# Kernel optimization log

Hardware: AMD Instinct MI355X
Metric: run time of the kernel (lower is better)

Reference implementation:

```python
import jax, jax.numpy as jnp
import numpy as np

D_IN = 4096
NUM_HEADS = 32
NUM_KV_GROUPS = 8
HEAD_DIM = D_IN // NUM_HEADS  # 128 (init overwrites head_dim)
GROUP_SIZE = NUM_HEADS // NUM_KV_GROUPS
SEQ = 2048
BATCH = 1
EPS = 1e-6


def layernorm(t, w, b):
    mu = jnp.mean(t, axis=-1, keepdims=True)
    var = jnp.var(t, axis=-1, keepdims=True)
    return (t - mu) * jax.lax.rsqrt(var + EPS) * w + b


def rope(t, cos, sin):
    # t: [B, H, S, D]; cos/sin: [S, D] broadcast over B, H
    half = t.shape[-1] // 2
    x1, x2 = t[..., :half], t[..., half:]
    rot = jnp.concatenate([-x2, x1], axis=-1)
    return t * cos + rot * sin


def setup_inputs() -> dict:
    key = jax.random.key(0)
    ks = jax.random.split(key, 10)
    x = jax.random.normal(ks[0], (BATCH, SEQ, D_IN), dtype=jnp.float32)
    mask = jnp.triu(jnp.ones((SEQ, SEQ), dtype=bool), k=1)  # True = masked (causal)
    # RoPE tables
    inv_freq = 1.0 / (10000.0 ** (np.arange(0, HEAD_DIM, 2, dtype=np.float32) / HEAD_DIM))
    pos = np.arange(SEQ, dtype=np.float32)
    ang = np.einsum('s,d->sd', pos, inv_freq)  # [S, D/2]
    ang = np.concatenate([ang, ang], axis=-1)  # [S, D]
    cos = jnp.asarray(np.cos(ang))
    sin = jnp.asarray(np.sin(ang))
    s = 0.02
    Wq = jax.random.normal(ks[1], (D_IN, NUM_HEADS * HEAD_DIM), dtype=jnp.float32) * s
    Wk = jax.random.normal(ks[2], (D_IN, NUM_KV_GROUPS * HEAD_DIM), dtype=jnp.float32) * s
    Wv = jax.random.normal(ks[3], (D_IN, NUM_KV_GROUPS * HEAD_DIM), dtype=jnp.float32) * s
    Wo = jax.random.normal(ks[4], (NUM_HEADS * HEAD_DIM, D_IN), dtype=jnp.float32) * s
    qn_w = jnp.ones((HEAD_DIM,), jnp.float32)
    qn_b = jnp.zeros((HEAD_DIM,), jnp.float32)
    kn_w = jnp.ones((HEAD_DIM,), jnp.float32)
    kn_b = jnp.zeros((HEAD_DIM,), jnp.float32)
    return {"x": x, "mask": mask, "cos": cos, "sin": sin, "Wq": Wq, "Wk": Wk,
            "Wv": Wv, "Wo": Wo, "qn_w": qn_w, "qn_b": qn_b, "kn_w": kn_w, "kn_b": kn_b}


def reference(x, mask, cos, sin, Wq, Wk, Wv, Wo, qn_w, qn_b, kn_w, kn_b):
    B, S, _ = x.shape
    q = (x @ Wq).reshape(B, S, NUM_HEADS, HEAD_DIM).transpose(0, 2, 1, 3)      # [B,H,S,D]
    k = (x @ Wk).reshape(B, S, NUM_KV_GROUPS, HEAD_DIM).transpose(0, 2, 1, 3)  # [B,G,S,D]
    v = (x @ Wv).reshape(B, S, NUM_KV_GROUPS, HEAD_DIM).transpose(0, 2, 1, 3)
    q = layernorm(q, qn_w, qn_b)
    k = layernorm(k, kn_w, kn_b)
    q = rope(q, cos, sin)
    k = rope(k, cos, sin)
    k = jnp.repeat(k, GROUP_SIZE, axis=1)  # [B,H,S,D]
    v = jnp.repeat(v, GROUP_SIZE, axis=1)
    scores = jnp.einsum('bhqd,bhkd->bhqk', q, k)
    scores = jnp.where(mask, -jnp.inf, scores)
    attn = jax.nn.softmax(scores / jnp.sqrt(jnp.float32(HEAD_DIM)), axis=-1)
    ctx = jnp.einsum('bhqk,bhkd->bhqd', attn, v)
    ctx = ctx.transpose(0, 2, 1, 3).reshape(B, S, NUM_HEADS * HEAD_DIM)
    return ctx @ Wo
```

## Files before the change

kernel.cpp:

```cpp
#include <hip/hip_runtime.h>
#include <stdint.h>

#define SQ   2048
#define DIN  4096
#define NH   32
#define NKV  8
#define HD   128
#define NQKV 6144

typedef float f32x4 __attribute__((ext_vector_type(4)));
typedef short bf16x8 __attribute__((ext_vector_type(8)));

__device__ __forceinline__ short f2bf(float f) {
  union { float f; uint32_t u; } v; v.f = f;
  uint32_t r = (v.u + 0x7FFFu + ((v.u >> 16) & 1u)) >> 16;
  return (short)r;
}

__device__ __forceinline__ void gl2lds(const void* g, void* l) {
  __builtin_amdgcn_global_load_lds(
      (const __attribute__((address_space(1))) void*)g,
      (__attribute__((address_space(3))) void*)l, 16, 0, 0);
}

__global__ void cvt_bf16(const float* __restrict__ src, short* __restrict__ dst, long n) {
  long i = ((long)blockIdx.x * blockDim.x + threadIdx.x) * 4;
  if (i + 3 < n) {
    float4 v = *(const float4*)(src + i);
    short o[4] = { f2bf(v.x), f2bf(v.y), f2bf(v.z), f2bf(v.w) };
    *(uint2*)(dst + i) = *(uint2*)o;
  }
}

__global__ __launch_bounds__(256) void transpose_cvt(const float* __restrict__ src, int ldS, long zS,
                                                     short* __restrict__ dst, int ldD, long zD) {
  __shared__ float tile[64][65];
  src += (long)blockIdx.z * zS;
  dst += (long)blockIdx.z * zD;
  int r0 = blockIdx.y * 64, c0 = blockIdx.x * 64;
  int tid = threadIdx.x;
#pragma unroll
  for (int i = 0; i < 16; ++i) {
    int idx = i * 256 + tid;
    int rr = idx >> 6, cc = idx & 63;
    tile[rr][cc] = src[(long)(r0 + rr) * ldS + c0 + cc];
  }
  __syncthreads();
#pragma unroll
  for (int i = 0; i < 16; ++i) {
    int idx = i * 256 + tid;
    int dr = idx >> 6, dc = idx & 63;
    dst[(long)(c0 + dr) * ldD + r0 + dc] = f2bf(tile[dc][dr]);
  }
}

#define HBUF  8192
#define BUFSZ 32768
#define MFMA(d, a, b) d = __builtin_amdgcn_mfma_f32_16x16x32_bf16(a, b, d, 0, 0, 0)

#define SA(t, h) { short* d = &lds[(((t) & 1) * BUFSZ) + (h) * HBUF + dA]; \
                   const short* s = aS + (long)(t) * 64 + (h) * 32;        \
                   gl2lds(s, d); gl2lds(s + K16, d + 512); }
#define SB(t, h) { short* d = &lds[(((t) & 1) * BUFSZ) + (h) * HBUF + dB]; \
                   const short* s = bS + (long)(t) * 64 + (h) * 32;        \
                   gl2lds(s, d); gl2lds(s + K16, d + 512); }

__global__ __launch_bounds__(512, 2) void gemm8p(const short* __restrict__ A, const short* __restrict__ Bt,
                                                 float* __restrict__ C, int M, int N, int K) {
  __shared__ __align__(16) short lds[2 * BUFSZ];
  int nwg = gridDim.x;
  int lin = ((int)blockIdx.x & 7) * (nwg >> 3) + ((int)blockIdx.x >> 3);
  int mt = M >> 8;
  int m0 = (lin % mt) << 8, n0 = (lin / mt) << 8;

  int tid = threadIdx.x;
  int w = tid >> 6, lane = tid & 63;
  int l16 = lane & 15, lq = lane >> 4;
  int wm = (w >> 2) << 7;
  int wn = (w & 3) << 6;

  int fl = (l16 & 3) ^ ((l16 >> 2) & 1);
  int aoff = (wm + l16) * 32 + ((lq ^ fl) << 3);
  int boff = 2 * HBUF + (wn + l16) * 32 + ((lq ^ fl) << 3);

  int grow = lane >> 2;
  int gch = (lane & 3) ^ ((grow & 3) ^ ((grow >> 2) & 1));
  const short* aS = A + (long)(m0 + 32 * w + grow) * K + gch * 8;
  const short* bS = Bt + (long)(n0 + 32 * w + grow) * K + gch * 8;
  long K16 = 16L * K;
  int dA = 1024 * w;
  int dB = 2 * HBUF + 1024 * w;

  f32x4 acc[8][4] = {};
  const int KT = K >> 6;

  SA(0, 0); SB(0, 0); SA(0, 1); SB(0, 1); SA(1, 0); SB(1, 0);
  asm volatile("s_waitcnt vmcnt(4)" ::: "memory");
  __builtin_amdgcn_s_barrier();

  for (int t = 0; t < KT; ++t) {
    const short* buf = &lds[(t & 1) * BUFSZ];
    bool s1 = (t + 1 < KT), s2 = (t + 2 < KT);
    bf16x8 af[8], bfr[4];

#pragma unroll
    for (int i = 0; i < 8; ++i) af[i] = *(const bf16x8*)&buf[aoff + i * 512];
    bfr[0] = *(const bf16x8*)&buf[boff];
    bfr[1] = *(const bf16x8*)&buf[boff + 512];
    if (s1) SA(t + 1, 1);
    __builtin_amdgcn_s_barrier();
    asm volatile("s_waitcnt lgkmcnt(0)" ::: "memory");
    __builtin_amdgcn_s_setprio(1);
#pragma unroll
    for (int i = 0; i < 8; ++i) { MFMA(acc[i][0], af[i], bfr[0]); MFMA(acc[i][1], af[i], bfr[1]); }
    __builtin_amdgcn_s_setprio(0);
    __builtin_amdgcn_s_barrier();

    bfr[2] = *(const bf16x8*)&buf[boff + 1024];
    bfr[3] = *(const bf16x8*)&buf[boff + 1536];
    if (s1) SB(t + 1, 1);
    __builtin_amdgcn_s_barrier();
    asm volatile("s_waitcnt lgkmcnt(0)" ::: "memory");
    __builtin_amdgcn_s_setprio(1);
#pragma unroll
    for (int i = 0; i < 8; ++i) { MFMA(acc[i][2], af[i], bfr[2]); MFMA(acc[i][3], af[i], bfr[3]); }
    __builtin_amdgcn_s_setprio(0);
    __builtin_amdgcn_s_barrier();

#pragma unroll
    for (int i = 0; i < 8; ++i) af[i] = *(const bf16x8*)&buf[HBUF + aoff + i * 512];
    bfr[2] = *(const bf16x8*)&buf[HBUF + boff + 1024];
    bfr[3] = *(const bf16x8*)&buf[HBUF + boff + 1536];
    if (s2) SA(t + 2, 0);
    __builtin_amdgcn_s_barrier();
    asm volatile("s_waitcnt lgkmcnt(0)" ::: "memory");
    __builtin_amdgcn_s_setprio(1);
#pragma unroll
    for (int i = 0; i < 8; ++i) { MFMA(acc[i][2], af[i], bfr[2]); MFMA(acc[i][3], af[i], bfr[3]); }
    __builtin_amdgcn_s_setprio(0);
    __builtin_amdgcn_s_barrier();

    bfr[0] = *(const bf16x8*)&buf[HBUF + boff];
    bfr[1] = *(const bf16x8*)&buf[HBUF + boff + 512];
    if (s2) SB(t + 2, 0);
    __builtin_amdgcn_s_barrier();
    asm volatile("s_waitcnt lgkmcnt(0)" ::: "memory");
    __builtin_amdgcn_s_setprio(1);
#pragma unroll
    for (int i = 0; i < 8; ++i) { MFMA(acc[i][0], af[i], bfr[0]); MFMA(acc[i][1], af[i], bfr[1]); }
    __builtin_amdgcn_s_setprio(0);
    if (t < KT - 1) {
      if (t == KT - 2) asm volatile("s_waitcnt vmcnt(0)" ::: "memory");
      else             asm volatile("s_waitcnt vmcnt(4)" ::: "memory");
      __builtin_amdgcn_s_barrier();
    }
  }

#pragma unroll
  for (int i = 0; i < 8; ++i)
#pragma unroll
    for (int j = 0; j < 4; ++j)
#pragma unroll
      for (int r = 0; r < 4; ++r)
        C[(long)(m0 + wm + i * 16 + lq * 4 + r) * N + n0 + wn + j * 16 + l16] = acc[i][j][r];
}

__global__ __launch_bounds__(64) void ln_rope(const float* __restrict__ qkv,
                                              const float* __restrict__ cosb, const float* __restrict__ sinb,
                                              const float* __restrict__ qw, const float* __restrict__ qb,
                                              const float* __restrict__ kw, const float* __restrict__ kb,
                                              short* __restrict__ qo, short* __restrict__ ko) {
  int s = blockIdx.x, slice = blockIdx.y, t = threadIdx.x;
  bool isq = slice < NH;
  int off = isq ? slice * HD : DIN + (slice - NH) * HD;
  const float* src = qkv + (long)s * NQKV + off;
  float v0 = src[t], v1 = src[t + 64];
  float sum = v0 + v1, ss = v0 * v0 + v1 * v1;
#pragma unroll
  for (int o = 1; o < 64; o <<= 1) { sum += __shfl_xor(sum, o); ss += __shfl_xor(ss, o); }
  float mu = sum * (1.f / 128.f);
  float var = ss * (1.f / 128.f) - mu * mu;
  float rstd = rsqrtf(var + 1e-6f);
  const float* w  = isq ? qw : kw;
  const float* bb = isq ? qb : kb;
  float n0 = (v0 - mu) * rstd * w[t]      + bb[t];
  float n1 = (v1 - mu) * rstd * w[t + 64] + bb[t + 64];
  float c0 = cosb[s * HD + t], c1 = cosb[s * HD + t + 64];
  float s0 = sinb[s * HD + t], s1 = sinb[s * HD + t + 64];
  float o0 = n0 * c0 - n1 * s0;
  float o1 = n1 * c1 + n0 * s1;
  short* dst = isq ? (qo + ((long)slice * SQ + s) * HD)
                   : (ko + ((long)(slice - NH) * SQ + s) * HD);
  dst[t] = f2bf(o0);
  dst[t + 64] = f2bf(o1);
}

__global__ __launch_bounds__(256) void attn(const short* __restrict__ q, const short* __restrict__ k,
                                            const short* __restrict__ vT, short* __restrict__ ctx) {
  int pair = blockIdx.x, h = blockIdx.y, g = h >> 2;
  int tid = threadIdx.x, w = tid >> 6, lane = tid & 63;
  int l16 = lane & 15, lq = lane >> 4;
  __shared__ __align__(16) short Ks[64 * 128];
  __shared__ __align__(16) short Vs[128 * 64];
  __shared__ __align__(16) short pbuf[4][16 * 72];
  const short* qh = q + (long)h * SQ * HD;
  const short* kg = k + (long)g * SQ * HD;
  const short* vg = vT + (long)g * HD * SQ;
  int kr = (w * 4) * 4 + (lane >> 4);
  int vrw = (w * 4) * 8 + (lane >> 3);
  const float sc = 0.08838834764831845f * 1.4426950408889634f;

  for (int st = 0; st < 2; ++st) {
    int qt = st ? (31 - pair) : pair;
    int qbase = qt * 64 + w * 16;
    bf16x8 aq[4];
#pragma unroll
    for (int kk = 0; kk < 4; ++kk)
      aq[kk] = *(const bf16x8*)&qh[(long)(qbase + l16) * HD + kk * 32 + lq * 8];
    float m_r[4], l_r[4];
    f32x4 acc[8] = {};
#pragma unroll
    for (int r = 0; r < 4; ++r) { m_r[r] = -__builtin_inff(); l_r[r] = 0.f; }

    for (int kt = 0; kt <= qt; ++kt) {
#pragma unroll
      for (int j = 0; j < 4; ++j) {
        int call = w * 4 + j;
        int r = kr + j * 4;
        int chk = (lane & 15) ^ (r & 15);
        gl2lds(&kg[(long)(kt * 64 + r) * HD + chk * 8], &Ks[call * 512]);
        int rv = vrw + j * 8;
        int chv = (lane & 7) ^ (rv & 7);
        gl2lds(&vg[(long)rv * SQ + kt * 64 + chv * 8], &Vs[call * 512]);
      }
      __syncthreads();
      f32x4 s4[4];
#pragma unroll
      for (int b = 0; b < 4; ++b) s4[b] = (f32x4){0.f, 0.f, 0.f, 0.f};
#pragma unroll
      for (int b = 0; b < 4; ++b) {
        int krow = b * 16 + l16;
#pragma unroll
        for (int kk = 0; kk < 4; ++kk) {
          bf16x8 bk = *(const bf16x8*)&Ks[krow * 128 + ((kk * 4 + lq) ^ (krow & 15)) * 8];
          s4[b] = __builtin_amdgcn_mfma_f32_16x16x32_bf16(aq[kk], bk, s4[b], 0, 0, 0);
        }
      }
      int qrow0 = qbase + lq * 4;
#pragma unroll
      for (int b = 0; b < 4; ++b) {
        int key = kt * 64 + b * 16 + l16;
#pragma unroll
        for (int r = 0; r < 4; ++r) {
          float val = s4[b][r] * sc;
          s4[b][r] = (key > qrow0 + r) ? -__builtin_inff() : val;
        }
      }
      float p[4][4];
#pragma unroll
      for (int r = 0; r < 4; ++r) {
        float mx = fmaxf(fmaxf(s4[0][r], s4[1][r]), fmaxf(s4[2][r], s4[3][r]));
#pragma unroll
        for (int o = 1; o < 16; o <<= 1) mx = fmaxf(mx, __shfl_xor(mx, o));
        float mnew = fmaxf(m_r[r], mx);
        float alpha = exp2f(m_r[r] - mnew);
        float sum = 0.f;
#pragma unroll
        for (int b = 0; b < 4; ++b) { float pv = exp2f(s4[b][r] - mnew); p[b][r] = pv; sum += pv; }
#pragma unroll
        for (int o = 1; o < 16; o <<= 1) sum += __shfl_xor(sum, o);
        l_r[r] = l_r[r] * alpha + sum;
        m_r[r] = mnew;
#pragma unroll
        for (int n = 0; n < 8; ++n) acc[n][r] *= alpha;
      }
#pragma unroll
      for (int b = 0; b < 4; ++b)
#pragma unroll
        for (int r = 0; r < 4; ++r)
          pbuf[w][(lq * 4 + r) * 72 + b * 16 + l16] = f2bf(p[b][r]);
#pragma unroll
      for (int kk = 0; kk < 2; ++kk) {
        bf16x8 pf = *(const bf16x8*)&pbuf[w][l16 * 72 + kk * 32 + lq * 8];
#pragma unroll
        for (int n = 0; n < 8; ++n) {
          int vrow = n * 16 + l16;
          bf16x8 vf = *(const bf16x8*)&Vs[vrow * 64 + ((kk * 4 + lq) ^ (vrow & 7)) * 8];
          acc[n] = __builtin_amdgcn_mfma_f32_16x16x32_bf16(pf, vf, acc[n], 0, 0, 0);
        }
      }
      __syncthreads();
    }
#pragma unroll
    for (int n = 0; n < 8; ++n)
#pragma unroll
      for (int r = 0; r < 4; ++r) {
        int srow = qbase + lq * 4 + r;
        ctx[(long)srow * (NH * HD) + h * HD + n * 16 + l16] = f2bf(acc[n][r] / l_r[r]);
      }
  }
}

#define XB_OFF     0L
#define QR_OFF     0L
#define WQKVT_OFF  16777216L
#define KR_OFF     16777216L
#define VT_OFF     20971520L
#define CTX_OFF    25165824L
#define WOT_OFF    67108864L
#define QKV_OFF    100663296L

extern "C" void kernel_launch(void* const* d_in, const int* in_sizes, int n_in,
                              void* d_out, int out_size, void* d_ws, size_t ws_size,
                              hipStream_t stream) {
  const float* x    = (const float*)d_in[0];
  const float* cosb = (const float*)d_in[2];
  const float* sinb = (const float*)d_in[3];
  const float* Wq   = (const float*)d_in[4];
  const float* Wk   = (const float*)d_in[5];
  const float* Wv   = (const float*)d_in[6];
  const float* Wo   = (const float*)d_in[7];
  const float* qnw  = (const float*)d_in[8];
  const float* qnb  = (const float*)d_in[9];
  const float* knw  = (const float*)d_in[10];
  const float* knb  = (const float*)d_in[11];

  char* ws = (char*)d_ws;
  short* xb    = (short*)(ws + XB_OFF);
  short* qr    = (short*)(ws + QR_OFF);
  short* wqkvt = (short*)(ws + WQKVT_OFF);
  short* krp   = (short*)(ws + KR_OFF);
  short* vt    = (short*)(ws + VT_OFF);
  short* ctx   = (short*)(ws + CTX_OFF);
  short* wot   = (short*)(ws + WOT_OFF);
  float* qkv   = (float*)(ws + QKV_OFF);

  cvt_bf16<<<8192, 256, 0, stream>>>(x, xb, (long)SQ * DIN);
  transpose_cvt<<<dim3(64, 64, 1), 256, 0, stream>>>(Wq, 4096, 0L, wqkvt, 4096, 0L);
  transpose_cvt<<<dim3(16, 64, 1), 256, 0, stream>>>(Wk, 1024, 0L, wqkvt + (long)4096 * 4096, 4096, 0L);
  transpose_cvt<<<dim3(16, 64, 1), 256, 0, stream>>>(Wv, 1024, 0L, wqkvt + (long)5120 * 4096, 4096, 0L);
  transpose_cvt<<<dim3(64, 64, 1), 256, 0, stream>>>(Wo, 4096, 0L, wot, 4096, 0L);
  gemm8p<<<(SQ / 256) * (NQKV / 256), 512, 0, stream>>>(xb, wqkvt, qkv, SQ, NQKV, DIN);
  ln_rope<<<dim3(SQ, NH + NKV), 64, 0, stream>>>(qkv, cosb, sinb, qnw, qnb, knw, knb, qr, krp);
  transpose_cvt<<<dim3(2, 32, 8), 256, 0, stream>>>(qkv + 5120, NQKV, 128L, vt, SQ, (long)HD * SQ);
  attn<<<dim3(16, NH), 256, 0, stream>>>(qr, krp, vt, ctx);
  gemm8p<<<(SQ / 256) * (DIN / 256), 512, 0, stream>>>(ctx, wot, (float*)d_out, SQ, DIN, DIN);
}
```

Before: 616.0 us.

## Switch GEMM LDS tiles to full 64-wide K rows with 8-way XOR swizzle

Replaces the split-half LDS layout (two 32-wide K halves per buffer) with full 64-element K rows per tile and an 8-chunk XOR swizzle, staging each K tile with four 16-byte global-to-LDS loads per thread. The prefetch schedule becomes a single tile ahead, waiting on vmcnt(0) at the end of each iteration, instead of staggered half-tile prefetches two steps ahead. The intent is to simplify addressing and reduce LDS bank conflicts on fragment reads. In exchange, less load latency is hidden because the staging depth drops.

```diff
diff --git a/kernel.cpp b/kernel.cpp
--- a/kernel.cpp
+++ b/kernel.cpp
@@ -54,16 +54,14 @@
   }
 }
 
-#define HBUF  8192
+#define ASZ   16384
 #define BUFSZ 32768
 #define MFMA(d, a, b) d = __builtin_amdgcn_mfma_f32_16x16x32_bf16(a, b, d, 0, 0, 0)
 
-#define SA(t, h) { short* d = &lds[(((t) & 1) * BUFSZ) + (h) * HBUF + dA]; \
-                   const short* s = aS + (long)(t) * 64 + (h) * 32;        \
-                   gl2lds(s, d); gl2lds(s + K16, d + 512); }
-#define SB(t, h) { short* d = &lds[(((t) & 1) * BUFSZ) + (h) * HBUF + dB]; \
-                   const short* s = bS + (long)(t) * 64 + (h) * 32;        \
-                   gl2lds(s, d); gl2lds(s + K16, d + 512); }
+#define SA(t) { short* d = &lds[(((t) & 1) * BUFSZ) + dA]; const short* s = aS + (long)(t) * 64; \
+                gl2lds(s, d); gl2lds(s + K8, d + 512); gl2lds(s + 2 * K8, d + 1024); gl2lds(s + 3 * K8, d + 1536); }
+#define SB(t) { short* d = &lds[(((t) & 1) * BUFSZ) + dB]; const short* s = bS + (long)(t) * 64; \
+                gl2lds(s, d); gl2lds(s + K8, d + 512); gl2lds(s + 2 * K8, d + 1024); gl2lds(s + 3 * K8, d + 1536); }
 
 __global__ __launch_bounds__(512, 2) void gemm8p(const short* __restrict__ A, const short* __restrict__ Bt,
                                                  float* __restrict__ C, int M, int N, int K) {
@@ -79,79 +77,78 @@
   int wm = (w >> 2) << 7;
   int wn = (w & 3) << 6;
 
-  int fl = (l16 & 3) ^ ((l16 >> 2) & 1);
-  int aoff = (wm + l16) * 32 + ((lq ^ fl) << 3);
-  int boff = 2 * HBUF + (wn + l16) * 32 + ((lq ^ fl) << 3);
-
-  int grow = lane >> 2;
-  int gch = (lane & 3) ^ ((grow & 3) ^ ((grow >> 2) & 1));
-  const short* aS = A + (long)(m0 + 32 * w + grow) * K + gch * 8;
-  const short* bS = Bt + (long)(n0 + 32 * w + grow) * K + gch * 8;
-  long K16 = 16L * K;
-  int dA = 1024 * w;
-  int dB = 2 * HBUF + 1024 * w;
+  int s7 = l16 & 7;
+  int fo0 = ((lq ^ s7) << 3);
+  int fo1 = (((lq + 4) ^ s7) << 3);
+  int arow = (wm + l16) * 64;
+  int brow = ASZ + (wn + l16) * 64;
+
+  int srow = lane >> 3;
+  int gch = (lane & 7) ^ srow;
+  const short* aS = A + (long)(m0 + 32 * w + srow) * K + gch * 8;
+  const short* bS = Bt + (long)(n0 + 32 * w + srow) * K + gch * 8;
+  long K8 = 8L * K;
+  int dA = (32 * w) * 64;
+  int dB = ASZ + (32 * w) * 64;
 
   f32x4 acc[8][4] = {};
   const int KT = K >> 6;
 
-  SA(0, 0); SB(0, 0); SA(0, 1); SB(0, 1); SA(1, 0); SB(1, 0);
-  asm volatile("s_waitcnt vmcnt(4)" ::: "memory");
+  SA(0); SB(0);
+  asm volatile("s_waitcnt vmcnt(0)" ::: "memory");
   __builtin_amdgcn_s_barrier();
 
   for (int t = 0; t < KT; ++t) {
     const short* buf = &lds[(t & 1) * BUFSZ];
-    bool s1 = (t + 1 < KT), s2 = (t + 2 < KT);
-    bf16x8 af[8], bfr[4];
-
-#pragma unroll
-    for (int i = 0; i < 8; ++i) af[i] = *(const bf16x8*)&buf[aoff + i * 512];
-    bfr[0] = *(const bf16x8*)&buf[boff];
-    bfr[1] = *(const bf16x8*)&buf[boff + 512];
-    if (s1) SA(t + 1, 1);
+    bool s1 = (t + 1 < KT);
+    bf16x8 af[8], b0, b1;
+
+#pragma unroll
+    for (int i = 0; i < 8; ++i) af[i] = *(const bf16x8*)&buf[arow + i * 1024 + fo0];
+    b0 = *(const bf16x8*)&buf[brow + fo0];
+    b1 = *(const bf16x8*)&buf[brow + 1024 + fo0];
+    if (s1) SA(t + 1);
     __builtin_amdgcn_s_barrier();
     asm volatile("s_waitcnt lgkmcnt(0)" ::: "memory");
     __builtin_amdgcn_s_setprio(1);
 #pragma unroll
-    for (int i = 0; i < 8; ++i) { MFMA(acc[i][0], af[i], bfr[0]); MFMA(acc[i][1], af[i], bfr[1]); }
+    for (int i = 0; i < 8; ++i) { MFMA(acc[i][0], af[i], b0); MFMA(acc[i][1], af[i], b1); }
     __builtin_amdgcn_s_setprio(0);
     __builtin_amdgcn_s_barrier();
 
-    bfr[2] = *(const bf16x8*)&buf[boff + 1024];
-    bfr[3] = *(const bf16x8*)&buf[boff + 1536];
-    if (s1) SB(t + 1, 1);
+    b0 = *(const bf16x8*)&buf[brow + 2048 + fo0];
+    b1 = *(const bf16x8*)&buf[brow + 3072 + fo0];
+    if (s1) SB(t + 1);
     __builtin_amdgcn_s_barrier();
     asm volatile("s_waitcnt lgkmcnt(0)" ::: "memory");
     __builtin_amdgcn_s_setprio(1);
 #pragma unroll
-    for (int i = 0; i < 8; ++i) { MFMA(acc[i][2], af[i], bfr[2]); MFMA(acc[i][3], af[i], bfr[3]); }
+    for (int i = 0; i < 8; ++i) { MFMA(acc[i][2], af[i], b0); MFMA(acc[i][3], af[i], b1); }
     __builtin_amdgcn_s_setprio(0);
     __builtin_amdgcn_s_barrier();
 
 #pragma unroll
-    for (int i = 0; i < 8; ++i) af[i] = *(const bf16x8*)&buf[HBUF + aoff + i * 512];
-    bfr[2] = *(const bf16x8*)&buf[HBUF + boff + 1024];
-    bfr[3] = *(const bf16x8*)&buf[HBUF + boff + 1536];
-    if (s2) SA(t + 2, 0);
+    for (int i = 0; i < 8; ++i) af[i] = *(const bf16x8*)&buf[arow + i * 1024 + fo1];
+    b0 = *(const bf16x8*)&buf[brow + 2048 + fo1];
+    b1 = *(const bf16x8*)&buf[brow + 3072 + fo1];
     __builtin_amdgcn_s_barrier();
     asm volatile("s_waitcnt lgkmcnt(0)" ::: "memory");
     __builtin_amdgcn_s_setprio(1);
 #pragma unroll
-    for (int i = 0; i < 8; ++i) { MFMA(acc[i][2], af[i], bfr[2]); MFMA(acc[i][3], af[i], bfr[3]); }
+    for (int i = 0; i < 8; ++i) { MFMA(acc[i][2], af[i], b0); MFMA(acc[i][3], af[i], b1); }
     __builtin_amdgcn_s_setprio(0);
     __builtin_amdgcn_s_barrier();
 
-    bfr[0] = *(const bf16x8*)&buf[HBUF + boff];
-    bfr[1] = *(const bf16x8*)&buf[HBUF + boff + 512];
-    if (s2) SB(t + 2, 0);
+    b0 = *(const bf16x8*)&buf[brow + fo1];
+    b1 = *(const bf16x8*)&buf[brow + 1024 + fo1];
     __builtin_amdgcn_s_barrier();
     asm volatile("s_waitcnt lgkmcnt(0)" ::: "memory");
     __builtin_amdgcn_s_setprio(1);
 #pragma unroll
-    for (int i = 0; i < 8; ++i) { MFMA(acc[i][0], af[i], bfr[0]); MFMA(acc[i][1], af[i], bfr[1]); }
+    for (int i = 0; i < 8; ++i) { MFMA(acc[i][0], af[i], b0); MFMA(acc[i][1], af[i], b1); }
     __builtin_amdgcn_s_setprio(0);
-    if (t < KT - 1) {
-      if (t == KT - 2) asm volatile("s_waitcnt vmcnt(0)" ::: "memory");
-      else             asm volatile("s_waitcnt vmcnt(4)" ::: "memory");
+    if (s1) {
+      asm volatile("s_waitcnt vmcnt(0)" ::: "memory");
       __builtin_amdgcn_s_barrier();
     }
   }
```

Result: faster. 598.4 us (-2.9%).
